# Kernel optimization log

Measured on AMD Instinct MI355X. Metric: run time of the kernel, lower is better.

## Reference

```python
import jax, jax.numpy as jnp
import numpy as np

KERNEL_MUL = 2.0
KERNEL_NUM = 5


def _mmd(source, target):
    n_s = source.shape[0]
    total = jnp.concatenate([source, target], axis=0)  # (2N, D)
    n = total.shape[0]
    # pairwise squared L2 via a^2 + b^2 - 2ab (avoids (2N,2N,D) intermediate)
    sq = jnp.sum(total * total, axis=1)  # (2N,)
    L2 = sq[:, None] + sq[None, :] - 2.0 * (total @ total.T)  # (2N, 2N)
    # torch uses L2_distance.data for bandwidth -> stop_gradient
    bandwidth = jax.lax.stop_gradient(jnp.sum(L2)) / (n * n - n)
    bandwidth = bandwidth / (KERNEL_MUL ** (KERNEL_NUM // 2))
    # multi-bandwidth RBF sum
    kernels = jnp.zeros_like(L2)
    for i in range(KERNEL_NUM):
        kernels = kernels + jnp.exp(-L2 / (bandwidth * KERNEL_MUL ** i))
    XX = kernels[:n_s, :n_s]
    YY = kernels[n_s:, n_s:]
    XY = kernels[:n_s, n_s:]
    YX = kernels[n_s:, :n_s]
    return jnp.mean(XX) + jnp.mean(YY) - jnp.mean(XY) - jnp.mean(YX)


def setup_inputs() -> dict:
    key = jax.random.key(0)
    k1, k2 = jax.random.split(key)
    source = jax.random.normal(k1, (4096, 256), dtype=jnp.float32)
    target = jax.random.normal(k2, (4096, 256), dtype=jnp.float32) + 0.5
    return {"source": source, "target": target}


def reference(source, target):
    return _mmd(source, target)
```

## Files before the change

kernel.cpp:

```cpp
#include <hip/hip_runtime.h>

typedef short bf16x8 __attribute__((ext_vector_type(8)));
typedef float f32x4 __attribute__((ext_vector_type(4)));
typedef float f32x16 __attribute__((ext_vector_type(16)));

#define KDIM 256
#define BT 128
#define BK 64

__device__ __forceinline__ unsigned short f2bf(float f) {
  unsigned u = __float_as_uint(f);
  unsigned r = (u + 0x7fffu + ((u >> 16) & 1u)) >> 16;
  return (unsigned short)r;
}
__device__ __forceinline__ float bf2f(unsigned short b) {
  return __uint_as_float(((unsigned)b) << 16);
}

__device__ __forceinline__ void async_cp16(const void* g, void* l) {
  __builtin_amdgcn_global_load_lds(
      (const __attribute__((address_space(1))) unsigned int*)g,
      (__attribute__((address_space(3))) unsigned int*)l, 16, 0, 0);
}

__global__ __launch_bounds__(256) void mmd_stage(
    const float* __restrict__ src, const float* __restrict__ tgt, int ns,
    unsigned short* __restrict__ Tbf, float* __restrict__ sq,
    float* __restrict__ scol, float* __restrict__ sum_sq,
    float* __restrict__ out) {
  __shared__ float sp[256];
  __shared__ float rw[4];
  int t = threadIdx.x;
  if (blockIdx.x == 0 && t == 0) out[0] = 0.f;
  int lane = t & 63, wave = t >> 6;
  sp[t] = 0.f;
  __syncthreads();
  int sub = t & 31;
  int rsel = t >> 5;
  float colacc[8];
#pragma unroll
  for (int j = 0; j < 8; ++j) colacc[j] = 0.f;
  float tsq = 0.f;
#pragma unroll
  for (int it = 0; it < 4; ++it) {
    int r = blockIdx.x * 32 + it * 8 + rsel;
    const float* rp = (r < ns) ? (src + (size_t)r * KDIM)
                               : (tgt + (size_t)(r - ns) * KDIM);
    float4 v0 = *(const float4*)(rp + sub * 8);
    float4 v1 = *(const float4*)(rp + sub * 8 + 4);
    float vals[8] = {v0.x, v0.y, v0.z, v0.w, v1.x, v1.y, v1.z, v1.w};
    unsigned pk[4];
    float ssp = 0.f;
#pragma unroll
    for (int j = 0; j < 4; ++j) {
      unsigned short b0 = f2bf(vals[2 * j]);
      unsigned short b1 = f2bf(vals[2 * j + 1]);
      float x0 = bf2f(b0), x1 = bf2f(b1);
      pk[j] = (unsigned)b0 | ((unsigned)b1 << 16);
      ssp += x0 * x0 + x1 * x1;
      colacc[2 * j] += x0;
      colacc[2 * j + 1] += x1;
    }
    *(uint4*)(Tbf + (size_t)r * KDIM + sub * 8) =
        make_uint4(pk[0], pk[1], pk[2], pk[3]);
    tsq += ssp;
    float ss = ssp;
#pragma unroll
    for (int off = 16; off; off >>= 1) ss += __shfl_down(ss, off, 32);
    if (sub == 0) sq[r] = ss;
  }
#pragma unroll
  for (int j = 0; j < 8; ++j) atomicAdd(&sp[sub * 8 + j], colacc[j]);
#pragma unroll
  for (int off = 32; off; off >>= 1) tsq += __shfl_down(tsq, off, 64);
  if (lane == 0) rw[wave] = tsq;
  __syncthreads();
  atomicAdd(&scol[t], sp[t]);
  if (t == 0) atomicAdd(sum_sq, rw[0] + rw[1] + rw[2] + rw[3]);
}

__device__ __forceinline__ float2 pk_add(float2 a, float2 b) {
  return make_float2(a.x + b.x, a.y + b.y);
}
__device__ __forceinline__ float2 pk_mul(float2 a, float2 b) {
  return make_float2(a.x * b.x, a.y * b.y);
}
__device__ __forceinline__ float2 pk_fma(float2 a, float2 b, float2 c) {
  return make_float2(__builtin_fmaf(a.x, b.x, c.x),
                     __builtin_fmaf(a.y, b.y, c.y));
}

__global__ __launch_bounds__(256) void mmd_main(
    const unsigned short* __restrict__ Tbf, const float* __restrict__ sq,
    const float* __restrict__ scol, const float* __restrict__ sum_sq,
    float* __restrict__ out, int n, int halfTiles, float inv) {
  __shared__ short As[BT * BK];
  __shared__ short Bs[BT * BK];
  __shared__ float sqa[BT];
  __shared__ float sqb[BT];
  __shared__ float red[4];
  __shared__ float s_c4;

  int id = blockIdx.x;
  int bi = (int)((sqrtf(8.f * (float)id + 1.f) - 1.f) * 0.5f);
  while ((bi + 1) * (bi + 2) / 2 <= id) ++bi;
  while (bi * (bi + 1) / 2 > id) --bi;
  int bj = id - bi * (bi + 1) / 2;
  int rowBase = bi * BT, colBase = bj * BT;

  int t = threadIdx.x;
  int lane = t & 63, wave = t >> 6;

  if (wave == 0) {
    float4 v = *(const float4*)(scol + lane * 4);
    float p = v.x * v.x + v.y * v.y + v.z * v.z + v.w * v.w;
#pragma unroll
    for (int off = 32; off; off >>= 1) p += __shfl_down(p, off, 64);
    if (lane == 0) {
      double ssq = (double)p, S = (double)sum_sq[0], nn = (double)n;
      double bwv = (2.0 * nn * S - 2.0 * ssq) / (nn * nn - nn) / 4.0;
      s_c4 = (float)(-1.4426950408889634 / (bwv * 16.0));
    }
  }

  if (t < 128) sqa[t] = sq[rowBase + t];
  else sqb[t - 128] = sq[colBase + (t - 128)];

  f32x16 acc[2][2];
#pragma unroll
  for (int a = 0; a < 2; ++a)
#pragma unroll
    for (int b = 0; b < 2; ++b)
#pragma unroll
      for (int e = 0; e < 16; ++e) acc[a][b][e] = 0.f;

  int wrow = (wave >> 1) * 64, wcol = (wave & 1) * 64;
  int lrow = lane >> 3;
  int kgsw = (lane & 7) ^ lrow;
  int frow = lane & 31;
  int khalf = lane >> 5;

  for (int c = 0; c < 4; ++c) {
    int k0 = c * BK;
#pragma unroll
    for (int j = 0; j < 4; ++j) {
      int R0 = j * 32 + wave * 8;
      int ldsoff = (j * 256 + wave * 64) * 8;
      async_cp16(Tbf + (size_t)(rowBase + R0 + lrow) * KDIM + k0 + kgsw * 8,
                 &As[ldsoff]);
      async_cp16(Tbf + (size_t)(colBase + R0 + lrow) * KDIM + k0 + kgsw * 8,
                 &Bs[ldsoff]);
    }
    __syncthreads();
#pragma unroll
    for (int ks = 0; ks < 4; ++ks) {
      int o = ks * 2 + khalf;
      bf16x8 af[2], bfv[2];
#pragma unroll
      for (int mt = 0; mt < 2; ++mt) {
        int r = wrow + mt * 32 + frow;
        int pg = o ^ (r & 7);
        af[mt] = *(const bf16x8*)&As[r * BK + pg * 8];
      }
#pragma unroll
      for (int nt = 0; nt < 2; ++nt) {
        int r = wcol + nt * 32 + frow;
        int pg = o ^ (r & 7);
        bfv[nt] = *(const bf16x8*)&Bs[r * BK + pg * 8];
      }
#pragma unroll
      for (int mt = 0; mt < 2; ++mt)
#pragma unroll
        for (int nt = 0; nt < 2; ++nt)
          acc[mt][nt] = __builtin_amdgcn_mfma_f32_32x32x16_bf16(
              af[mt], bfv[nt], acc[mt][nt], 0, 0, 0);
    }
    __syncthreads();
  }

  float c4 = s_c4;
  float m2c4 = -2.f * c4;
  float2 m2v = make_float2(m2c4, m2c4);
  int rb = khalf * 4;
  float2 lsum2 = make_float2(0.f, 0.f);
#pragma unroll
  for (int mt = 0; mt < 2; ++mt) {
    f32x4 rq[4];
#pragma unroll
    for (int q = 0; q < 4; ++q)
      rq[q] = *(const f32x4*)&sqa[wrow + mt * 32 + 8 * q + rb];
#pragma unroll
    for (int nt = 0; nt < 2; ++nt) {
      float cb = sqb[wcol + nt * 32 + frow] * c4;
#pragma unroll
      for (int q = 0; q < 4; ++q) {
#pragma unroll
        for (int s = 0; s < 4; s += 2) {
          float2 g =
              make_float2(acc[mt][nt][q * 4 + s], acc[mt][nt][q * 4 + s + 1]);
          float2 sab = make_float2(rq[q][s] * c4 + cb, rq[q][s + 1] * c4 + cb);
          float2 u = pk_fma(g, m2v, sab);
          float2 e = make_float2(__builtin_amdgcn_exp2f(u.x),
                                 __builtin_amdgcn_exp2f(u.y));
          float2 e2 = pk_mul(e, e);
          float2 e4 = pk_mul(e2, e2);
          float2 e8 = pk_mul(e4, e4);
          float2 sm = pk_add(e, e2);
          sm = pk_add(sm, e4);
          sm = pk_add(sm, e8);
          sm = pk_fma(e8, e8, sm);
          lsum2 = pk_add(lsum2, sm);
        }
      }
    }
  }
  float lsum = lsum2.x + lsum2.y;
#pragma unroll
  for (int off = 32; off; off >>= 1) lsum += __shfl_down(lsum, off, 64);
  if (lane == 0) red[wave] = lsum;
  __syncthreads();
  if (t == 0) {
    float w = ((bi < halfTiles) == (bj < halfTiles)) ? 1.f : -1.f;
    float f = (bi == bj) ? 1.f : 2.f;
    atomicAdd(out, w * f * inv * (red[0] + red[1] + red[2] + red[3]));
  }
}

extern "C" void kernel_launch(void* const* d_in, const int* in_sizes, int n_in,
                              void* d_out, int out_size, void* d_ws,
                              size_t ws_size, hipStream_t stream) {
  const float* src = (const float*)d_in[0];
  const float* tgt = (const float*)d_in[1];
  int ns = in_sizes[0] / KDIM;
  int ntr = in_sizes[1] / KDIM;
  int n = ns + ntr;

  char* ws = (char*)d_ws;
  unsigned short* Tbf = (unsigned short*)ws;
  size_t off = (size_t)n * KDIM * sizeof(unsigned short);
  float* sq = (float*)(ws + off);     off += (size_t)n * 4;
  float* scol = (float*)(ws + off);   off += (size_t)KDIM * 4;
  float* sum_sq = (float*)(ws + off);

  hipMemsetAsync(scol, 0, (KDIM + 1) * sizeof(float), stream);

  mmd_stage<<<n / 32, 256, 0, stream>>>(src, tgt, ns, Tbf, sq, scol, sum_sq,
                                        (float*)d_out);

  int nb = n / BT;
  int nblk = nb * (nb + 1) / 2;
  mmd_main<<<nblk, 256, 0, stream>>>(Tbf, sq, scol, sum_sq, (float*)d_out, n,
                                     ns / BT, 1.f / ((float)ns * (float)ns));
}
```

Before: 118.3 us.

## Double-buffer K chunks with async LDS loads and switch to 16x16x32 MFMA

The main GEMM+exp kernel now splits K into 8 chunks of 32 with double-buffered LDS, issuing the next chunk's global-to-LDS copies before computing the current one. Explicit vmcnt waits and raw barriers replace __syncthreads. It also switches from 32x32x16 to 16x16x32 MFMA tiles with a new LDS swizzle, reads the squared norms directly from global memory instead of staging them in LDS, and adds an occupancy hint of 4 blocks per CU. The aim is to hide load latency and raise occupancy, at the cost of more barriers and manual waitcnt handling that could be fragile.

```diff
diff --git a/kernel.cpp b/kernel.cpp
--- a/kernel.cpp
+++ b/kernel.cpp
@@ -2,11 +2,11 @@
 
 typedef short bf16x8 __attribute__((ext_vector_type(8)));
 typedef float f32x4 __attribute__((ext_vector_type(4)));
-typedef float f32x16 __attribute__((ext_vector_type(16)));
 
 #define KDIM 256
 #define BT 128
-#define BK 64
+#define BK 32
+#define NC 8
 
 __device__ __forceinline__ unsigned short f2bf(float f) {
   unsigned u = __float_as_uint(f);
@@ -90,14 +90,17 @@
                      __builtin_fmaf(a.y, b.y, c.y));
 }
 
-__global__ __launch_bounds__(256) void mmd_main(
+#define BAR() __builtin_amdgcn_s_barrier()
+#define LGKM0() asm volatile("s_waitcnt lgkmcnt(0)" ::: "memory")
+#define VMC4() asm volatile("s_waitcnt vmcnt(4)" ::: "memory")
+#define VMC0() asm volatile("s_waitcnt vmcnt(0)" ::: "memory")
+
+__global__ __launch_bounds__(256, 4) void mmd_main(
     const unsigned short* __restrict__ Tbf, const float* __restrict__ sq,
     const float* __restrict__ scol, const float* __restrict__ sum_sq,
     float* __restrict__ out, int n, int halfTiles, float inv) {
-  __shared__ short As[BT * BK];
-  __shared__ short Bs[BT * BK];
-  __shared__ float sqa[BT];
-  __shared__ float sqb[BT];
+  __shared__ short As[2][BT * BK];
+  __shared__ short Bs[2][BT * BK];
   __shared__ float red[4];
   __shared__ float s_c4;
 
@@ -121,96 +124,117 @@
       double bwv = (2.0 * nn * S - 2.0 * ssq) / (nn * nn - nn) / 4.0;
       s_c4 = (float)(-1.4426950408889634 / (bwv * 16.0));
     }
-  }
-
-  if (t < 128) sqa[t] = sq[rowBase + t];
-  else sqb[t - 128] = sq[colBase + (t - 128)];
-
-  f32x16 acc[2][2];
-#pragma unroll
-  for (int a = 0; a < 2; ++a)
-#pragma unroll
-    for (int b = 0; b < 2; ++b)
-#pragma unroll
-      for (int e = 0; e < 16; ++e) acc[a][b][e] = 0.f;
+    LGKM0();
+  }
+
+  int srow = wave * 16 + (lane >> 2);
+  int g0 = ((lane & 3) - (srow >> 1)) & 3;
+  int g1 = ((lane & 3) - ((srow + 64) >> 1)) & 3;
+  int ldsb0 = wave * 512;
+  int ldsb1 = wave * 512 + 2048;
 
   int wrow = (wave >> 1) * 64, wcol = (wave & 1) * 64;
-  int lrow = lane >> 3;
-  int kgsw = (lane & 7) ^ lrow;
-  int frow = lane & 31;
-  int khalf = lane >> 5;
-
-  for (int c = 0; c < 4; ++c) {
+  int frow = lane & 15;
+  int kq = lane >> 4;
+
+  auto stage = [&](int c) {
     int k0 = c * BK;
-#pragma unroll
-    for (int j = 0; j < 4; ++j) {
-      int R0 = j * 32 + wave * 8;
-      int ldsoff = (j * 256 + wave * 64) * 8;
-      async_cp16(Tbf + (size_t)(rowBase + R0 + lrow) * KDIM + k0 + kgsw * 8,
-                 &As[ldsoff]);
-      async_cp16(Tbf + (size_t)(colBase + R0 + lrow) * KDIM + k0 + kgsw * 8,
-                 &Bs[ldsoff]);
-    }
-    __syncthreads();
-#pragma unroll
-    for (int ks = 0; ks < 4; ++ks) {
-      int o = ks * 2 + khalf;
-      bf16x8 af[2], bfv[2];
-#pragma unroll
-      for (int mt = 0; mt < 2; ++mt) {
-        int r = wrow + mt * 32 + frow;
-        int pg = o ^ (r & 7);
-        af[mt] = *(const bf16x8*)&As[r * BK + pg * 8];
-      }
-#pragma unroll
-      for (int nt = 0; nt < 2; ++nt) {
-        int r = wcol + nt * 32 + frow;
-        int pg = o ^ (r & 7);
-        bfv[nt] = *(const bf16x8*)&Bs[r * BK + pg * 8];
-      }
-#pragma unroll
-      for (int mt = 0; mt < 2; ++mt)
-#pragma unroll
-        for (int nt = 0; nt < 2; ++nt)
-          acc[mt][nt] = __builtin_amdgcn_mfma_f32_32x32x16_bf16(
-              af[mt], bfv[nt], acc[mt][nt], 0, 0, 0);
-    }
-    __syncthreads();
+    short* Ad = As[c & 1];
+    short* Bd = Bs[c & 1];
+    async_cp16(Tbf + (size_t)(rowBase + srow) * KDIM + k0 + g0 * 8, Ad + ldsb0);
+    async_cp16(Tbf + (size_t)(rowBase + srow + 64) * KDIM + k0 + g1 * 8,
+               Ad + ldsb1);
+    async_cp16(Tbf + (size_t)(colBase + srow) * KDIM + k0 + g0 * 8, Bd + ldsb0);
+    async_cp16(Tbf + (size_t)(colBase + srow + 64) * KDIM + k0 + g1 * 8,
+               Bd + ldsb1);
+  };
+
+  f32x4 acc[4][4];
+#pragma unroll
+  for (int a = 0; a < 4; ++a)
+#pragma unroll
+    for (int b = 0; b < 4; ++b) {
+      f32x4 z = {0.f, 0.f, 0.f, 0.f};
+      acc[a][b] = z;
+    }
+
+  stage(0);
+
+#pragma unroll
+  for (int c = 0; c < NC; ++c) {
+    if (c < NC - 1) {
+      stage(c + 1);
+      VMC4();
+    } else {
+      VMC0();
+    }
+    BAR();
+
+    const short* Ab = As[c & 1];
+    const short* Bb = Bs[c & 1];
+    bf16x8 af[4], bfv[4];
+#pragma unroll
+    for (int mt = 0; mt < 4; ++mt) {
+      int r = wrow + mt * 16 + frow;
+      int s = (kq + (r >> 1)) & 3;
+      af[mt] = *(const bf16x8*)&Ab[r * BK + s * 8];
+    }
+#pragma unroll
+    for (int nt = 0; nt < 4; ++nt) {
+      int r = wcol + nt * 16 + frow;
+      int s = (kq + (r >> 1)) & 3;
+      bfv[nt] = *(const bf16x8*)&Bb[r * BK + s * 8];
+    }
+#pragma unroll
+    for (int mt = 0; mt < 4; ++mt)
+#pragma unroll
+      for (int nt = 0; nt < 4; ++nt)
+        acc[mt][nt] = __builtin_amdgcn_mfma_f32_16x16x32_bf16(
+            af[mt], bfv[nt], acc[mt][nt], 0, 0, 0);
+    BAR();
   }
 
   float c4 = s_c4;
   float m2c4 = -2.f * c4;
   float2 m2v = make_float2(m2c4, m2c4);
-  int rb = khalf * 4;
+  int ccol = lane & 15;
+  int rb = (lane >> 4) * 4;
+  float ra[16];
+#pragma unroll
+  for (int mt = 0; mt < 4; ++mt) {
+    float4 rv = *(const float4*)(sq + rowBase + wrow + mt * 16 + rb);
+    ra[mt * 4 + 0] = rv.x * c4;
+    ra[mt * 4 + 1] = rv.y * c4;
+    ra[mt * 4 + 2] = rv.z * c4;
+    ra[mt * 4 + 3] = rv.w * c4;
+  }
+  float cbv[4];
+#pragma unroll
+  for (int nt = 0; nt < 4; ++nt)
+    cbv[nt] = sq[colBase + wcol + nt * 16 + ccol] * c4;
+
   float2 lsum2 = make_float2(0.f, 0.f);
 #pragma unroll
-  for (int mt = 0; mt < 2; ++mt) {
-    f32x4 rq[4];
-#pragma unroll
-    for (int q = 0; q < 4; ++q)
-      rq[q] = *(const f32x4*)&sqa[wrow + mt * 32 + 8 * q + rb];
-#pragma unroll
-    for (int nt = 0; nt < 2; ++nt) {
-      float cb = sqb[wcol + nt * 32 + frow] * c4;
-#pragma unroll
-      for (int q = 0; q < 4; ++q) {
-#pragma unroll
-        for (int s = 0; s < 4; s += 2) {
-          float2 g =
-              make_float2(acc[mt][nt][q * 4 + s], acc[mt][nt][q * 4 + s + 1]);
-          float2 sab = make_float2(rq[q][s] * c4 + cb, rq[q][s + 1] * c4 + cb);
-          float2 u = pk_fma(g, m2v, sab);
-          float2 e = make_float2(__builtin_amdgcn_exp2f(u.x),
-                                 __builtin_amdgcn_exp2f(u.y));
-          float2 e2 = pk_mul(e, e);
-          float2 e4 = pk_mul(e2, e2);
-          float2 e8 = pk_mul(e4, e4);
-          float2 sm = pk_add(e, e2);
-          sm = pk_add(sm, e4);
-          sm = pk_add(sm, e8);
-          sm = pk_fma(e8, e8, sm);
-          lsum2 = pk_add(lsum2, sm);
-        }
+  for (int mt = 0; mt < 4; ++mt) {
+#pragma unroll
+    for (int nt = 0; nt < 4; ++nt) {
+      float cb = cbv[nt];
+#pragma unroll
+      for (int rp = 0; rp < 4; rp += 2) {
+        float2 g = make_float2(acc[mt][nt][rp], acc[mt][nt][rp + 1]);
+        float2 sab =
+            make_float2(ra[mt * 4 + rp] + cb, ra[mt * 4 + rp + 1] + cb);
+        float2 u = pk_fma(g, m2v, sab);
+        float2 e = make_float2(__builtin_amdgcn_exp2f(u.x),
+                               __builtin_amdgcn_exp2f(u.y));
+        float2 e2 = pk_mul(e, e);
+        float2 e4 = pk_mul(e2, e2);
+        float2 e8 = pk_mul(e4, e4);
+        float2 sm = pk_add(e, e2);
+        sm = pk_add(sm, e4);
+        sm = pk_add(sm, e8);
+        sm = pk_fma(e8, e8, sm);
+        lsum2 = pk_add(lsum2, sm);
       }
     }
   }
```

New measurement: 116.4 us. No clear change (-1.6%).
